# Kernel optimization log

Measured on AMD Instinct MI355X. Metric: run time of the kernel, lower is better.

The kernel has to match this reference:

```python
import jax, jax.numpy as jnp
import numpy as np

WINDOW_SIZE = 11
CHANNEL = 3
SIGMA = 1.5
C1 = 0.01 ** 2
C2 = 0.03 ** 2


def _create_window(window_size, channel, dtype=jnp.float32):
    x = np.arange(window_size)
    g = np.exp(-((x - window_size // 2) ** 2) / (2.0 * SIGMA ** 2)).astype(np.float32)
    g = g / g.sum()
    w2d = np.outer(g, g)  # [ws, ws]
    # depthwise kernel: [channel, 1, ws, ws] (OIHW with groups=channel)
    w = np.broadcast_to(w2d, (channel, 1, window_size, window_size))
    return jnp.asarray(w, dtype=dtype)


def _dwconv(x, window):
    pad = WINDOW_SIZE // 2
    return jax.lax.conv_general_dilated(
        x, window,
        window_strides=(1, 1),
        padding=[(pad, pad), (pad, pad)],
        dimension_numbers=("NCHW", "OIHW", "NCHW"),
        feature_group_count=x.shape[1],
    )


def setup_inputs() -> dict:
    key = jax.random.key(0)
    k1, k2 = jax.random.split(key)
    img1 = jax.random.uniform(k1, (16, 3, 512, 512), dtype=jnp.float32)
    img2 = jax.random.uniform(k2, (16, 3, 512, 512), dtype=jnp.float32)
    return {"img1": img1, "img2": img2}


def reference(img1, img2):
    window = _create_window(WINDOW_SIZE, img1.shape[1], img1.dtype)
    mu1 = _dwconv(img1, window)
    mu2 = _dwconv(img2, window)
    mu1_sq = mu1 * mu1
    mu2_sq = mu2 * mu2
    mu1_mu2 = mu1 * mu2
    sigma1_sq = _dwconv(img1 * img1, window) - mu1_sq
    sigma2_sq = _dwconv(img2 * img2, window) - mu2_sq
    sigma12 = _dwconv(img1 * img2, window) - mu1_mu2
    ssim_map = ((2 * mu1_mu2 + C1) * (2 * sigma12 + C2)) / (
        (mu1_sq + mu2_sq + C1) * (sigma1_sq + sigma2_sq + C2)
    )
    return 1 - ssim_map.mean()
```

## Files before the change

kernel.cpp:

```cpp
#include <hip/hip_runtime.h>


typedef __attribute__((ext_vector_type(8))) short bf16x8;
typedef __attribute__((ext_vector_type(4))) float f32x4;
typedef __attribute__((ext_vector_type(2))) float f32x2;
typedef __attribute__((ext_vector_type(2))) __bf16 bfx2;

constexpr int TX   = 64;
constexpr int BY   = 256;
constexpr int IMW  = 512;
constexpr int IMH  = 512;
constexpr int NPL  = 48;
constexpr int GX   = IMW / TX;
constexpr int GYB  = IMH / BY;
constexpr int NBLK = GX * GYB * NPL;
constexpr int NCH  = BY / 16;
constexpr int CB   = 12288;
constexpr float C1c = 0.01f * 0.01f;
constexpr float C2c = 0.03f * 0.03f;

union frag {
    bf16x8 f;
    unsigned int u[4];
    uint4 q;
};

__device__ __forceinline__ unsigned int pk_bf16(float lo, float hi) {
    unsigned int a = __float_as_uint(lo);
    unsigned int b = __float_as_uint(hi);
    a += 0x7FFFu + ((a >> 16) & 1u);
    b += 0x7FFFu + ((b >> 16) & 1u);
    return (b & 0xFFFF0000u) | (a >> 16);
}

__device__ __forceinline__ unsigned int pk_rne(float lo, float hi) {
    f32x2 v; v.x = lo; v.y = hi;
    bfx2 b = __builtin_convertvector(v, bfx2);
    return *reinterpret_cast<unsigned int*>(&b);
}

__device__ __forceinline__ float wsel(int d) {
    float w = 0.f;
    w = (d == 0 || d == 10) ? 0.00102838f : w;
    w = (d == 1 || d == 9)  ? 0.00759876f : w;
    w = (d == 2 || d == 8)  ? 0.03600077f : w;
    w = (d == 3 || d == 7)  ? 0.10936082f : w;
    w = (d == 4 || d == 6)  ? 0.21300553f : w;
    w = (d == 5)            ? 0.26601171f : w;
    return w;
}

__global__ void ssim_weight_setup(unsigned int* __restrict__ wbuf)
{
    const int lane = threadIdx.x & 63;
    const int ln   = lane & 15;
    const int lg   = lane >> 4;
#pragma unroll
    for (int w = 0; w < 4; ++w) {
        const int ka = lg * 8 + 2 * w;
        wbuf[lane * 8 + w] = pk_bf16(wsel(ka - ln - 3), wsel(ka + 1 - ln - 3));
        const int j0  = 2 * w;
        const int wr0 = (j0 < 4) ? (lg * 4 + j0) : (12 + lg * 4 + j0);
        wbuf[lane * 8 + 4 + w] = pk_bf16(wsel(wr0 - ln - 3), wsel(wr0 + 1 - ln - 3));
    }
}

template<int OFF>
__device__ __forceinline__ void cstep(const char* lds, int ro0, int ro1, bool ok,
                                      const frag& whf,
                                      uint2* __restrict__ D)
{
    float4 ra0 = *reinterpret_cast<const float4*>(lds + OFF + ro0);
    float4 ra1 = *reinterpret_cast<const float4*>(lds + OFF + ro1);
    float4 rb0 = *reinterpret_cast<const float4*>(lds + OFF + CB / 2 + ro0);
    float4 rb1 = *reinterpret_cast<const float4*>(lds + OFF + CB / 2 + ro1);
    const float4 zz = make_float4(0.f, 0.f, 0.f, 0.f);
    if (!ok) { ra0 = zz; ra1 = zz; rb0 = zz; rb1 = zz; }

    const f32x4 z = {0.f, 0.f, 0.f, 0.f};
    frag fa, fb, faa, fbb, fab;
    fa.u[0]  = pk_rne(ra0.x, ra0.y);               fb.u[0]  = pk_rne(rb0.x, rb0.y);
    faa.u[0] = pk_rne(ra0.x*ra0.x, ra0.y*ra0.y);
    fbb.u[0] = pk_rne(rb0.x*rb0.x, rb0.y*rb0.y);
    fab.u[0] = pk_rne(ra0.x*rb0.x, ra0.y*rb0.y);
    fa.u[1]  = pk_rne(ra0.z, ra0.w);               fb.u[1]  = pk_rne(rb0.z, rb0.w);
    faa.u[1] = pk_rne(ra0.z*ra0.z, ra0.w*ra0.w);
    fbb.u[1] = pk_rne(rb0.z*rb0.z, rb0.w*rb0.w);
    fab.u[1] = pk_rne(ra0.z*rb0.z, ra0.w*rb0.w);
    fa.u[2]  = pk_rne(ra1.x, ra1.y);               fb.u[2]  = pk_rne(rb1.x, rb1.y);
    faa.u[2] = pk_rne(ra1.x*ra1.x, ra1.y*ra1.y);
    fbb.u[2] = pk_rne(rb1.x*rb1.x, rb1.y*rb1.y);
    fab.u[2] = pk_rne(ra1.x*rb1.x, ra1.y*rb1.y);
    fa.u[3]  = pk_rne(ra1.z, ra1.w);               fb.u[3]  = pk_rne(rb1.z, rb1.w);
    faa.u[3] = pk_rne(ra1.z*ra1.z, ra1.w*ra1.w);
    fbb.u[3] = pk_rne(rb1.z*rb1.z, rb1.w*rb1.w);
    fab.u[3] = pk_rne(ra1.z*rb1.z, ra1.w*rb1.w);

    f32x4 d;
    d = __builtin_amdgcn_mfma_f32_16x16x32_bf16(fa.f,  whf.f, z, 0, 0, 0);
    D[0] = make_uint2(pk_rne(d[0], d[1]), pk_rne(d[2], d[3]));
    d = __builtin_amdgcn_mfma_f32_16x16x32_bf16(fb.f,  whf.f, z, 0, 0, 0);
    D[1] = make_uint2(pk_rne(d[0], d[1]), pk_rne(d[2], d[3]));
    d = __builtin_amdgcn_mfma_f32_16x16x32_bf16(faa.f, whf.f, z, 0, 0, 0);
    D[2] = make_uint2(pk_rne(d[0], d[1]), pk_rne(d[2], d[3]));
    d = __builtin_amdgcn_mfma_f32_16x16x32_bf16(fbb.f, whf.f, z, 0, 0, 0);
    D[3] = make_uint2(pk_rne(d[0], d[1]), pk_rne(d[2], d[3]));
    d = __builtin_amdgcn_mfma_f32_16x16x32_bf16(fab.f, whf.f, z, 0, 0, 0);
    D[4] = make_uint2(pk_rne(d[0], d[1]), pk_rne(d[2], d[3]));
}

__device__ __forceinline__ void vstep(const frag& whv,
                                      const uint2* __restrict__ Dp,
                                      const uint2* __restrict__ Dc,
                                      float& lsum)
{
    const f32x4 z = {0.f, 0.f, 0.f, 0.f};
    f32x4 res[5];
#pragma unroll
    for (int p = 0; p < 5; ++p) {
        frag Bf;
        Bf.u[0] = Dp[p].x; Bf.u[1] = Dp[p].y;
        Bf.u[2] = Dc[p].x; Bf.u[3] = Dc[p].y;
        res[p] = __builtin_amdgcn_mfma_f32_16x16x32_bf16(whv.f, Bf.f, z, 0, 0, 0);
    }
#pragma unroll
    for (int j = 0; j < 4; ++j) {
        const float mu1 = res[0][j];
        const float mu2 = res[1][j];
        const float m1s = mu1 * mu1;
        const float m2s = mu2 * mu2;
        const float m12 = mu1 * mu2;
        const float s11 = res[2][j] - m1s;
        const float s22 = res[3][j] - m2s;
        const float s12 = res[4][j] - m12;
        const float num = (2.f * m12 + C1c) * (2.f * s12 + C2c);
        const float den = (m1s + m2s + C1c) * (s11 + s22 + C2c);
        lsum = fmaf(num, __builtin_amdgcn_rcpf(den), lsum);
    }
}

__global__ __launch_bounds__(256, 3)
void ssim_mfma(const float* __restrict__ img1, const float* __restrict__ img2,
               const unsigned int* __restrict__ wbuf,
               float* __restrict__ partials)
{
    const int tid  = threadIdx.x;
    const int lane = tid & 63;
    const int wave = tid >> 6;
    const int ln   = lane & 15;
    const int lg   = lane >> 4;

    const int h    = blockIdx.x;
    const int xcd  = h & 7;
    const int slot = h >> 3;
    const int pr   = xcd * 12 + (slot >> 3);
    const int bx   = slot & 7;
    const int by   = pr & 1;
    const int bz   = pr >> 1;

    const int y0   = by * BY;
    const float* __restrict__ p1 = img1 + (size_t)bz * (IMW * IMH);
    const float* __restrict__ p2 = img2 + (size_t)bz * (IMW * IMH);

    frag whf, whv;
    whf.q = reinterpret_cast<const uint4*>(wbuf)[lane * 2];
    whv.q = reinterpret_cast<const uint4*>(wbuf)[lane * 2 + 1];

    __shared__ __align__(16) char lds[4 * CB];
    __shared__ float wsum[4];

    const int Lp0 = tid;
    const int rw0 = Lp0 / 24;
    int sg0 = (Lp0 % 24) - rw0; sg0 += (sg0 < 0) ? 24 : 0;
    int cc0 = bx * TX - 16 + 4 * sg0; cc0 = cc0 < 0 ? 0 : (cc0 > IMW - 4 ? IMW - 4 : cc0);
    const float* gb0 = p1;

    const int L1  = tid + 256;
    const int Lp1 = (L1 < 384) ? L1 : (L1 - 384);
    const int rw1 = Lp1 / 24;
    int sg1 = (Lp1 % 24) - rw1; sg1 += (sg1 < 0) ? 24 : 0;
    int cc1 = bx * TX - 16 + 4 * sg1; cc1 = cc1 < 0 ? 0 : (cc1 > IMW - 4 ? IMW - 4 : cc1);
    const float* gb1 = (L1 < 384) ? p1 : p2;

    const int Lp2 = tid + 512 - 384;
    const int rw2 = Lp2 / 24;
    int sg2 = (Lp2 % 24) - rw2; sg2 += (sg2 < 0) ? 24 : 0;
    int cc2 = bx * TX - 16 + 4 * sg2; cc2 = cc2 < 0 ? 0 : (cc2 > IMW - 4 ? IMW - 4 : cc2);
    const float* gb2 = p2;

    const int wbase = wave * 1024;

    const int s0  = 4 * wave + 2 + 2 * lg;
    const int rk0 = (s0 + ln) % 24;
    const int rk1 = (s0 + 1 + ln) % 24;
    const int ro0 = (ln * 24 + rk0) * 16;
    const int ro1 = (ln * 24 + rk1) * 16;
    const int cbase = bx * TX + wave * 16 - 8 + lg * 8;
    const bool colok = ((unsigned)cbase <= (unsigned)(IMW - 8));

    uint2 DA[5], DB[5];
    float lsum = 0.f;

#define CLMP(r) ((r) < 0 ? 0 : ((r) > IMH - 1 ? IMH - 1 : (r)))
#define ISSUE(c, OFF) do{ \
    const int i0 = CLMP(y0 + 16 * (c) - 8 + rw0); \
    const int i1 = CLMP(y0 + 16 * (c) - 8 + rw1); \
    const int i2 = CLMP(y0 + 16 * (c) - 8 + rw2); \
    __builtin_amdgcn_global_load_lds( \
        (const __attribute__((address_space(1))) void*)(gb0 + (size_t)i0 * IMW + cc0), \
        (__attribute__((address_space(3))) void*)(lds + (OFF) + wbase), 16, 0, 0); \
    __builtin_amdgcn_global_load_lds( \
        (const __attribute__((address_space(1))) void*)(gb1 + (size_t)i1 * IMW + cc1), \
        (__attribute__((address_space(3))) void*)(lds + (OFF) + 4096 + wbase), 16, 0, 0); \
    __builtin_amdgcn_global_load_lds( \
        (const __attribute__((address_space(1))) void*)(gb2 + (size_t)i2 * IMW + cc2), \
        (__attribute__((address_space(3))) void*)(lds + (OFF) + 8192 + wbase), 16, 0, 0); \
    } while (0)
#define VMW(n) do{ \
    asm volatile("s_waitcnt vmcnt(" #n ")" ::: "memory"); \
    __builtin_amdgcn_sched_barrier(0); } while (0)
#define BAR() do{ \
    __builtin_amdgcn_sched_barrier(0); \
    __builtin_amdgcn_s_barrier(); \
    __builtin_amdgcn_sched_barrier(0); } while (0)
#define ROWOK(c) (colok && ((unsigned)(y0 + 16 * (c) - 8 + ln) < (unsigned)IMH))

    ISSUE(0, 0 * CB);
    ISSUE(1, 1 * CB);
    ISSUE(2, 2 * CB);
    VMW(6);
    BAR();
    cstep<0 * CB>(lds, ro0, ro1, ROWOK(0), whf, DA);

    for (int u = 0; u < 3; ++u) {
        const int c0 = 4 * u;
        ISSUE(c0 + 3, 3 * CB); VMW(6); BAR();
        cstep<1 * CB>(lds, ro0, ro1, ROWOK(c0 + 1), whf, DB);
        vstep(whv, DA, DB, lsum);
        ISSUE(c0 + 4, 0 * CB); VMW(6); BAR();
        cstep<2 * CB>(lds, ro0, ro1, ROWOK(c0 + 2), whf, DA);
        vstep(whv, DB, DA, lsum);
        ISSUE(c0 + 5, 1 * CB); VMW(6); BAR();
        cstep<3 * CB>(lds, ro0, ro1, ROWOK(c0 + 3), whf, DB);
        vstep(whv, DA, DB, lsum);
        ISSUE(c0 + 6, 2 * CB); VMW(6); BAR();
        cstep<0 * CB>(lds, ro0, ro1, ROWOK(c0 + 4), whf, DA);
        vstep(whv, DB, DA, lsum);
    }
    ISSUE(15, 3 * CB); VMW(6); BAR();
    cstep<1 * CB>(lds, ro0, ro1, ROWOK(13), whf, DB);
    vstep(whv, DA, DB, lsum);
    ISSUE(16, 0 * CB); VMW(6); BAR();
    cstep<2 * CB>(lds, ro0, ro1, ROWOK(14), whf, DA);
    vstep(whv, DB, DA, lsum);
    VMW(3); BAR();
    cstep<3 * CB>(lds, ro0, ro1, ROWOK(15), whf, DB);
    vstep(whv, DA, DB, lsum);
    VMW(0); BAR();
    cstep<0 * CB>(lds, ro0, ro1, ROWOK(16), whf, DA);
    vstep(whv, DB, DA, lsum);
#undef CLMP
#undef ISSUE
#undef VMW
#undef BAR
#undef ROWOK

#pragma unroll
    for (int off = 32; off > 0; off >>= 1)
        lsum += __shfl_down(lsum, off, 64);

    if (lane == 0) wsum[wave] = lsum;
    __syncthreads();
    if (tid == 0) {
        float tot = wsum[0] + wsum[1] + wsum[2] + wsum[3];
        const int bid = (bz * GYB + by) * GX + bx;
        partials[bid] = tot;
    }
}

__global__ __launch_bounds__(256)
void ssim_reduce_kernel(const float* __restrict__ partials,
                        float* __restrict__ out)
{
    __shared__ double sm[256];
    double s = 0.0;
    for (int i = threadIdx.x; i < NBLK; i += 256) s += (double)partials[i];
    sm[threadIdx.x] = s;
    __syncthreads();
    for (int stride = 128; stride > 0; stride >>= 1) {
        if (threadIdx.x < stride) sm[threadIdx.x] += sm[threadIdx.x + stride];
        __syncthreads();
    }
    if (threadIdx.x == 0) {
        double mean = sm[0] / (double)((size_t)NPL * IMW * IMH);
        out[0] = (float)(1.0 - mean);
    }
}

extern "C" void kernel_launch(void* const* d_in, const int* in_sizes, int n_in,
                              void* d_out, int out_size, void* d_ws, size_t ws_size,
                              hipStream_t stream)
{
    (void)in_sizes; (void)n_in; (void)out_size; (void)ws_size;
    const float* img1 = (const float*)d_in[0];
    const float* img2 = (const float*)d_in[1];
    float* out = (float*)d_out;

    unsigned int* wbuf = (unsigned int*)d_ws;
    float* partials = (float*)((char*)d_ws + 4096);

    ssim_weight_setup<<<1, 64, 0, stream>>>(wbuf);
    ssim_mfma<<<dim3(NBLK), 256, 0, stream>>>(img1, img2, wbuf, partials);
    ssim_reduce_kernel<<<1, 256, 0, stream>>>(partials, out);
}
```

Baseline: 33.26 us.

## Prefetch next chunk's LDS reads into registers one step ahead

Splits the column step into an LDS read phase and a compute phase. The next chunk's float4 values are read from LDS one iteration early, so LDS latency overlaps with the current chunk's MFMA and vertical work. To keep that buffer ready, the vmcnt waits are tightened from 6 to 3, which means one more chunk of global loads must land before each barrier. This cuts the depth of global prefetch and adds eight float4 registers per thread, which may raise register pressure.

```diff
diff --git a/kernel.cpp b/kernel.cpp
--- a/kernel.cpp
+++ b/kernel.cpp
@@ -65,15 +65,11 @@
     }
 }
 
-template<int OFF>
-__device__ __forceinline__ void cstep(const char* lds, int ro0, int ro1, bool ok,
-                                      const frag& whf,
-                                      uint2* __restrict__ D)
-{
-    float4 ra0 = *reinterpret_cast<const float4*>(lds + OFF + ro0);
-    float4 ra1 = *reinterpret_cast<const float4*>(lds + OFF + ro1);
-    float4 rb0 = *reinterpret_cast<const float4*>(lds + OFF + CB / 2 + ro0);
-    float4 rb1 = *reinterpret_cast<const float4*>(lds + OFF + CB / 2 + ro1);
+__device__ __forceinline__ void cstepR(float4 ra0, float4 ra1,
+                                       float4 rb0, float4 rb1, bool ok,
+                                       const frag& whf,
+                                       uint2* __restrict__ D)
+{
     const float4 zz = make_float4(0.f, 0.f, 0.f, 0.f);
     if (!ok) { ra0 = zz; ra1 = zz; rb0 = zz; rb1 = zz; }
 
@@ -199,6 +195,8 @@
     const bool colok = ((unsigned)cbase <= (unsigned)(IMW - 8));
 
     uint2 DA[5], DB[5];
+    float4 xA0, xA1, xA2, xA3;
+    float4 xB0, xB1, xB2, xB3;
     float lsum = 0.f;
 
 #define CLMP(r) ((r) < 0 ? 0 : ((r) > IMH - 1 ? IMH - 1 : (r)))
@@ -224,46 +222,60 @@
     __builtin_amdgcn_s_barrier(); \
     __builtin_amdgcn_sched_barrier(0); } while (0)
 #define ROWOK(c) (colok && ((unsigned)(y0 + 16 * (c) - 8 + ln) < (unsigned)IMH))
+#define RD(OFF, X0, X1, X2, X3) do{ \
+    X0 = *reinterpret_cast<const float4*>(lds + (OFF) + ro0); \
+    X1 = *reinterpret_cast<const float4*>(lds + (OFF) + ro1); \
+    X2 = *reinterpret_cast<const float4*>(lds + (OFF) + CB / 2 + ro0); \
+    X3 = *reinterpret_cast<const float4*>(lds + (OFF) + CB / 2 + ro1); } while (0)
 
     ISSUE(0, 0 * CB);
     ISSUE(1, 1 * CB);
     ISSUE(2, 2 * CB);
-    VMW(6);
+    VMW(3);
     BAR();
-    cstep<0 * CB>(lds, ro0, ro1, ROWOK(0), whf, DA);
+    RD(0 * CB, xA0, xA1, xA2, xA3);
+    RD(1 * CB, xB0, xB1, xB2, xB3);
+    cstepR(xA0, xA1, xA2, xA3, ROWOK(0), whf, DA);
 
     for (int u = 0; u < 3; ++u) {
         const int c0 = 4 * u;
-        ISSUE(c0 + 3, 3 * CB); VMW(6); BAR();
-        cstep<1 * CB>(lds, ro0, ro1, ROWOK(c0 + 1), whf, DB);
+        ISSUE(c0 + 3, 3 * CB); VMW(3); BAR();
+        RD(2 * CB, xA0, xA1, xA2, xA3);
+        cstepR(xB0, xB1, xB2, xB3, ROWOK(c0 + 1), whf, DB);
         vstep(whv, DA, DB, lsum);
-        ISSUE(c0 + 4, 0 * CB); VMW(6); BAR();
-        cstep<2 * CB>(lds, ro0, ro1, ROWOK(c0 + 2), whf, DA);
+        ISSUE(c0 + 4, 0 * CB); VMW(3); BAR();
+        RD(3 * CB, xB0, xB1, xB2, xB3);
+        cstepR(xA0, xA1, xA2, xA3, ROWOK(c0 + 2), whf, DA);
         vstep(whv, DB, DA, lsum);
-        ISSUE(c0 + 5, 1 * CB); VMW(6); BAR();
-        cstep<3 * CB>(lds, ro0, ro1, ROWOK(c0 + 3), whf, DB);
+        ISSUE(c0 + 5, 1 * CB); VMW(3); BAR();
+        RD(0 * CB, xA0, xA1, xA2, xA3);
+        cstepR(xB0, xB1, xB2, xB3, ROWOK(c0 + 3), whf, DB);
         vstep(whv, DA, DB, lsum);
-        ISSUE(c0 + 6, 2 * CB); VMW(6); BAR();
-        cstep<0 * CB>(lds, ro0, ro1, ROWOK(c0 + 4), whf, DA);
+        ISSUE(c0 + 6, 2 * CB); VMW(3); BAR();
+        RD(1 * CB, xB0, xB1, xB2, xB3);
+        cstepR(xA0, xA1, xA2, xA3, ROWOK(c0 + 4), whf, DA);
         vstep(whv, DB, DA, lsum);
     }
-    ISSUE(15, 3 * CB); VMW(6); BAR();
-    cstep<1 * CB>(lds, ro0, ro1, ROWOK(13), whf, DB);
+    ISSUE(15, 3 * CB); VMW(3); BAR();
+    RD(2 * CB, xA0, xA1, xA2, xA3);
+    cstepR(xB0, xB1, xB2, xB3, ROWOK(13), whf, DB);
     vstep(whv, DA, DB, lsum);
-    ISSUE(16, 0 * CB); VMW(6); BAR();
-    cstep<2 * CB>(lds, ro0, ro1, ROWOK(14), whf, DA);
+    ISSUE(16, 0 * CB); VMW(3); BAR();
+    RD(3 * CB, xB0, xB1, xB2, xB3);
+    cstepR(xA0, xA1, xA2, xA3, ROWOK(14), whf, DA);
     vstep(whv, DB, DA, lsum);
-    VMW(3); BAR();
-    cstep<3 * CB>(lds, ro0, ro1, ROWOK(15), whf, DB);
+    VMW(0); BAR();
+    RD(0 * CB, xA0, xA1, xA2, xA3);
+    cstepR(xB0, xB1, xB2, xB3, ROWOK(15), whf, DB);
     vstep(whv, DA, DB, lsum);
-    VMW(0); BAR();
-    cstep<0 * CB>(lds, ro0, ro1, ROWOK(16), whf, DA);
+    cstepR(xA0, xA1, xA2, xA3, ROWOK(16), whf, DA);
     vstep(whv, DB, DA, lsum);
 #undef CLMP
 #undef ISSUE
 #undef VMW
 #undef BAR
 #undef ROWOK
+#undef RD
 
 #pragma unroll
     for (int off = 32; off > 0; off >>= 1)
```

After: 35.70 us. +7.3%, slower.

## Fuse weight setup and final reduction into main SSIM kernel

Applied to the files above, without the earlier changes.

Computes the bf16 MFMA weight fragments inline in each thread instead of loading them from a buffer filled by a separate setup kernel. Replaces the separate reduce kernel with a double atomicAdd per block plus a completion counter, where the last block writes the final result. This trades three launches for a memset plus one launch, removing inter-kernel gaps at the cost of atomic contention and extra per-thread weight ALU work.

```diff
diff --git a/kernel.cpp b/kernel.cpp
--- a/kernel.cpp
+++ b/kernel.cpp
@@ -48,21 +48,6 @@
     w = (d == 4 || d == 6)  ? 0.21300553f : w;
     w = (d == 5)            ? 0.26601171f : w;
     return w;
-}
-
-__global__ void ssim_weight_setup(unsigned int* __restrict__ wbuf)
-{
-    const int lane = threadIdx.x & 63;
-    const int ln   = lane & 15;
-    const int lg   = lane >> 4;
-#pragma unroll
-    for (int w = 0; w < 4; ++w) {
-        const int ka = lg * 8 + 2 * w;
-        wbuf[lane * 8 + w] = pk_bf16(wsel(ka - ln - 3), wsel(ka + 1 - ln - 3));
-        const int j0  = 2 * w;
-        const int wr0 = (j0 < 4) ? (lg * 4 + j0) : (12 + lg * 4 + j0);
-        wbuf[lane * 8 + 4 + w] = pk_bf16(wsel(wr0 - ln - 3), wsel(wr0 + 1 - ln - 3));
-    }
 }
 
 template<int OFF>
@@ -141,8 +126,8 @@
 
 __global__ __launch_bounds__(256, 3)
 void ssim_mfma(const float* __restrict__ img1, const float* __restrict__ img2,
-               const unsigned int* __restrict__ wbuf,
-               float* __restrict__ partials)
+               double* __restrict__ acc, unsigned int* __restrict__ cnt,
+               float* __restrict__ out)
 {
     const int tid  = threadIdx.x;
     const int lane = tid & 63;
@@ -163,8 +148,14 @@
     const float* __restrict__ p2 = img2 + (size_t)bz * (IMW * IMH);
 
     frag whf, whv;
-    whf.q = reinterpret_cast<const uint4*>(wbuf)[lane * 2];
-    whv.q = reinterpret_cast<const uint4*>(wbuf)[lane * 2 + 1];
+#pragma unroll
+    for (int w = 0; w < 4; ++w) {
+        const int ka = lg * 8 + 2 * w;
+        whf.u[w] = pk_bf16(wsel(ka - ln - 3), wsel(ka + 1 - ln - 3));
+        const int j0  = 2 * w;
+        const int wr0 = (j0 < 4) ? (lg * 4 + j0) : (12 + lg * 4 + j0);
+        whv.u[w] = pk_bf16(wsel(wr0 - ln - 3), wsel(wr0 + 1 - ln - 3));
+    }
 
     __shared__ __align__(16) char lds[4 * CB];
     __shared__ float wsum[4];
@@ -273,27 +264,14 @@
     __syncthreads();
     if (tid == 0) {
         float tot = wsum[0] + wsum[1] + wsum[2] + wsum[3];
-        const int bid = (bz * GYB + by) * GX + bx;
-        partials[bid] = tot;
-    }
-}
-
-__global__ __launch_bounds__(256)
-void ssim_reduce_kernel(const float* __restrict__ partials,
-                        float* __restrict__ out)
-{
-    __shared__ double sm[256];
-    double s = 0.0;
-    for (int i = threadIdx.x; i < NBLK; i += 256) s += (double)partials[i];
-    sm[threadIdx.x] = s;
-    __syncthreads();
-    for (int stride = 128; stride > 0; stride >>= 1) {
-        if (threadIdx.x < stride) sm[threadIdx.x] += sm[threadIdx.x + stride];
-        __syncthreads();
-    }
-    if (threadIdx.x == 0) {
-        double mean = sm[0] / (double)((size_t)NPL * IMW * IMH);
-        out[0] = (float)(1.0 - mean);
+        atomicAdd(acc, (double)tot);
+        __threadfence();
+        unsigned int old = atomicAdd(cnt, 1u);
+        if (old == (unsigned int)(NBLK - 1)) {
+            double sum = atomicAdd(acc, 0.0);
+            double mean = sum / (double)((size_t)NPL * IMW * IMH);
+            out[0] = (float)(1.0 - mean);
+        }
     }
 }
 
@@ -306,10 +284,9 @@
     const float* img2 = (const float*)d_in[1];
     float* out = (float*)d_out;
 
-    unsigned int* wbuf = (unsigned int*)d_ws;
-    float* partials = (float*)((char*)d_ws + 4096);
-
-    ssim_weight_setup<<<1, 64, 0, stream>>>(wbuf);
-    ssim_mfma<<<dim3(NBLK), 256, 0, stream>>>(img1, img2, wbuf, partials);
-    ssim_reduce_kernel<<<1, 256, 0, stream>>>(partials, out);
-}
+    double* acc = (double*)d_ws;
+    unsigned int* cnt = (unsigned int*)((char*)d_ws + 8);
+
+    hipMemsetAsync(d_ws, 0, 16, stream);
+    ssim_mfma<<<dim3(NBLK), 256, 0, stream>>>(img1, img2, acc, cnt, out);
+}
```

Measured after the change: 49.85 us. 49.9% more time.
